# Optimization experiments

Hardware: AMD Instinct MI355X
Metric: run time of the kernel (lower is better)

Reference implementation:

```python
import jax, jax.numpy as jnp
import numpy as np
from jax import lax

B, T, C_IN, HW = 16, 2048, 17, 8
N_CONV, HID, OUT = 4, 150, 2
IN_SZ = N_CONV * 6 * 6  # 144


def setup_inputs() -> dict:
    key = jax.random.key(0)
    ks = jax.random.split(key, 9)
    s = lambda *sh: 1.0 / np.sqrt(sh[-1])
    return {
        "inputs": jax.random.normal(ks[0], (B, T, C_IN, HW, HW), jnp.float32),
        "conv_w": jax.random.normal(ks[1], (N_CONV, C_IN, 3, 3), jnp.float32) * 0.1,
        "conv_b": jax.random.normal(ks[2], (N_CONV,), jnp.float32) * 0.1,
        "w_ih": jax.random.normal(ks[3], (4 * HID, IN_SZ), jnp.float32) * s(IN_SZ),
        "w_hh": jax.random.normal(ks[4], (4 * HID, HID), jnp.float32) * s(HID),
        "b_ih": jax.random.normal(ks[5], (4 * HID,), jnp.float32) * s(HID),
        "b_hh": jax.random.normal(ks[6], (4 * HID,), jnp.float32) * s(HID),
        "last_w": jax.random.normal(ks[7], (OUT, HID), jnp.float32) * s(HID),
        "last_b": jax.random.normal(ks[8], (OUT,), jnp.float32) * s(HID),
    }


def reference(inputs, conv_w, conv_b, w_ih, w_hh, b_ih, b_hh, last_w, last_b):
    b, t = inputs.shape[:2]
    # Conv2d over all timesteps at once (same math as the per-step loop).
    x = inputs.reshape(b * t, C_IN, HW, HW)
    y = lax.conv_general_dilated(
        x, conv_w, window_strides=(1, 1), padding="VALID",
        dimension_numbers=("NCHW", "OIHW", "NCHW"),
    ) + conv_b[None, :, None, None]           # [B*T, 4, 6, 6]
    y = jax.nn.relu(y).reshape(b, t, IN_SZ)   # [B, T, 144]
    # Precompute input-to-gate projection for every step (batched GEMM).
    gates_x = jnp.einsum("btf,gf->btg", y, w_ih) + b_ih + b_hh  # [B, T, 600]

    def step(carry, gx):
        h, c = carry
        g = gx + h @ w_hh.T  # [B, 600]; PyTorch gate order: i, f, g, o
        i, f, gg, o = jnp.split(g, 4, axis=-1)
        c = jax.nn.sigmoid(f) * c + jax.nn.sigmoid(i) * jnp.tanh(gg)
        h = jax.nn.sigmoid(o) * jnp.tanh(c)
        return (h, c), None

    h0 = jnp.zeros((b, HID), inputs.dtype)
    (hT, _), _ = lax.scan(step, (h0, h0), jnp.swapaxes(gates_x, 0, 1))
    return hT @ last_w.T + last_b  # [B, 2] == last(h_T).squeeze()
```

## Files before the change

kernel.cpp:

```cpp
#include <hip/hip_runtime.h>

typedef _Float16 f16;
typedef _Float16 f16x4 __attribute__((ext_vector_type(4)));
typedef _Float16 f16x8 __attribute__((ext_vector_type(8)));
typedef float f32x4 __attribute__((ext_vector_type(4)));
typedef int i32x4 __attribute__((ext_vector_type(4)));

#define TLEN 2048
#define TPAD 2050
#define NCOL 640
#define GSTEP (16 * NCOL)
#define SPITCH 1100
#define K1 1.4426950408889634f
#define K2 2.8853900817779268f

__global__ __launch_bounds__(512, 1) void conv_gemm(
    const float* __restrict__ inp, const float* __restrict__ cw,
    const float* __restrict__ cb,
    const float* __restrict__ w_ih, const float* __restrict__ b_ih,
    const float* __restrict__ b_hh,
    f16* __restrict__ gates3)
{
    __shared__ __align__(16) float s_in[16][SPITCH];
    __shared__ __align__(16) f16 s_y[8][16][168];
    __shared__ float s_w[612];
    const int tid = threadIdx.x, w = tid >> 6, lane = tid & 63;
    const int col = lane & 15, grp = lane >> 4;
    for (int i = tid; i < 612; i += 512) s_w[i] = cw[i];

    f16x8 bfr[5][5];
    float bb[5];
    #pragma unroll
    for (int i = 0; i < 5; ++i) {
        const int colg = (w * 5 + i) * 16 + col;
        const int u = colg >> 2, G = colg & 3;
        const float sc = (G == 2) ? K2 : -K1;
        const bool valid = (u < 150);
        const int row = valid ? G * 150 + u : 0;
        #pragma unroll
        for (int kt = 0; kt < 5; ++kt) {
            const int k0 = kt * 32 + grp * 8;
            f16x8 v;
            #pragma unroll
            for (int e = 0; e < 8; ++e) v[e] = (f16)0.f;
            if (valid && k0 < 144) {
                const float* p = w_ih + (size_t)row * 144 + k0;
                #pragma unroll
                for (int e = 0; e < 8; ++e) v[e] = (f16)(p[e] * sc);
            }
            bfr[i][kt] = v;
        }
        bb[i] = valid ? (b_ih[row] + b_hh[row]) * sc : 0.f;
    }

    const int cb_b = tid & 15, unit = tid >> 4;
    const int oc = unit / 6, oy = unit % 6;
    const float cbias = (unit < 24) ? cb[oc] : 0.f;
    __syncthreads();

    const int t0 = blockIdx.x * 8;
    for (int tl = 0; tl < 8; ++tl) {
        const int t = t0 + tl;
        __syncthreads();
        {
            const int si = tid >> 5, l2 = tid & 31;
            const float4* ip =
                (const float4*)(inp + ((size_t)si * TLEN + t) * 1088);
            for (int k = l2; k < 272; k += 32)
                *(float4*)(&s_in[si][k * 4]) = ip[k];
        }
        __syncthreads();
        if (unit < 24) {
            const float* wp = s_w + oc * 153;
            float acc[6] = {cbias, cbias, cbias, cbias, cbias, cbias};
            #pragma unroll 1
            for (int ic = 0; ic < 17; ++ic) {
                #pragma unroll
                for (int ky = 0; ky < 3; ++ky) {
                    const float* r = &s_in[cb_b][ic * 64 + (oy + ky) * 8];
                    const float4 f0 = *(const float4*)r;
                    const float4 f1 = *(const float4*)(r + 4);
                    const float w0 = wp[ic * 9 + ky * 3 + 0];
                    const float w1 = wp[ic * 9 + ky * 3 + 1];
                    const float w2 = wp[ic * 9 + ky * 3 + 2];
                    acc[0] += f0.x * w0 + f0.y * w1 + f0.z * w2;
                    acc[1] += f0.y * w0 + f0.z * w1 + f0.w * w2;
                    acc[2] += f0.z * w0 + f0.w * w1 + f1.x * w2;
                    acc[3] += f0.w * w0 + f1.x * w1 + f1.y * w2;
                    acc[4] += f1.x * w0 + f1.y * w1 + f1.z * w2;
                    acc[5] += f1.y * w0 + f1.z * w1 + f1.w * w2;
                }
            }
            #pragma unroll
            for (int ox = 0; ox < 6; ++ox)
                s_y[tl][cb_b][oc * 36 + oy * 6 + ox] = (f16)fmaxf(acc[ox], 0.f);
        } else if (unit == 24) {
            #pragma unroll
            for (int k = 0; k < 16; ++k) s_y[tl][cb_b][144 + k] = (f16)0.f;
        }
    }
    __syncthreads();
    for (int tl = 0; tl < 8; ++tl) {
        const int t = t0 + tl;
        f16x8 a[5];
        #pragma unroll
        for (int kt = 0; kt < 5; ++kt)
            a[kt] = *(const f16x8*)(&s_y[tl][col][kt * 32 + grp * 8]);
        #pragma unroll
        for (int i = 0; i < 5; ++i) {
            f32x4 acc = {0.f, 0.f, 0.f, 0.f};
            #pragma unroll
            for (int kt = 0; kt < 5; ++kt)
                acc = __builtin_amdgcn_mfma_f32_16x16x32_f16(a[kt], bfr[i][kt], acc, 0, 0, 0);
            const int colg = (w * 5 + i) * 16 + col;
            #pragma unroll
            for (int r = 0; r < 4; ++r)
                gates3[((size_t)(t * 16 + grp * 4 + r)) * NCOL + colg] =
                    (f16)(acc[r] + bb[i]);
        }
    }
}

__device__ __forceinline__ void lstm_stepQ(
    int t, int cur, f16x4& pfu, f16x4& pfc, const f16*& pLoad,
    const i32x4 (&afrag)[5][3], const f32x4& scv,
    signed char* hqs, f16* hfs, float& cst,
    int grp, int sel, bool wr, int u)
{
    const f16x4 pnew = *(const f16x4*)pLoad;
    pLoad += GSTEP;

    const signed char* hr = hqs + cur * 192 + grp * 16;
    i32x4 bf[3];
    #pragma unroll
    for (int kt = 0; kt < 3; ++kt)
        bf[kt] = *(const i32x4*)(hr + kt * 64);

    float gx0 = (float)pfu[0], gx1 = (float)pfu[1];
    float gx2 = (float)pfu[2], gx3 = (float)pfu[3];
    pfc = pnew;

    const i32x4 zc = {0, 0, 0, 0};
    i32x4 acc[5];
    #pragma unroll
    for (int i = 0; i < 5; ++i)
        acc[i] = __builtin_amdgcn_mfma_i32_16x16x64_i8(afrag[i][0], bf[0], zc, 0, 0, 0);
    #pragma unroll
    for (int kt = 1; kt < 3; ++kt)
        #pragma unroll
        for (int i = 0; i < 5; ++i)
            acc[i] = __builtin_amdgcn_mfma_i32_16x16x64_i8(afrag[i][kt], bf[kt], acc[i], 0, 0, 0);

    int s0 = acc[0][0], s1 = acc[0][1], s2 = acc[0][2], s3 = acc[0][3];
    #pragma unroll
    for (int i = 1; i < 5; ++i) {
        const bool p = (sel == i);
        s0 = p ? acc[i][0] : s0;
        s1 = p ? acc[i][1] : s1;
        s2 = p ? acc[i][2] : s2;
        s3 = p ? acc[i][3] : s3;
    }

    const float g0 = fmaf((float)s0, scv[0], gx0);
    const float g1 = fmaf((float)s1, scv[1], gx1);
    const float g2 = fmaf((float)s2, scv[2], gx2);
    const float g3 = fmaf((float)s3, scv[3], gx3);

    const float ei = __builtin_amdgcn_exp2f(g0);
    const float ef = __builtin_amdgcn_exp2f(g1);
    const float eg = __builtin_amdgcn_exp2f(fminf(g2, 38.f));
    const float eo = __builtin_amdgcn_exp2f(g3);
    const float dig = (1.f + ei) * (eg + 1.f);
    const float c = cst * __builtin_amdgcn_rcpf(1.f + ef)
                  + (eg - 1.f) * __builtin_amdgcn_rcpf(dig);
    cst = c;
    const float ec = __builtin_amdgcn_exp2f(fminf(K2 * c, 80.f));
    const float h = (ec - 1.f) * __builtin_amdgcn_rcpf((1.f + eo) * (ec + 1.f));

    if (wr) hqs[(cur ^ 1) * 192 + u] = (signed char)(int)rintf(127.f * h);
    if (t == TLEN - 1 && wr) hfs[u] = (f16)h;

    asm volatile("s_waitcnt lgkmcnt(0)" ::: "memory");
    __builtin_amdgcn_s_barrier();
    __builtin_amdgcn_sched_barrier(0);
}

__global__ __launch_bounds__(512, 1) void lstm_scan(
    const f16* __restrict__ gates3, const float* __restrict__ w_hh,
    const float* __restrict__ last_w, const float* __restrict__ last_b,
    float* __restrict__ out)
{
    __shared__ __align__(16) signed char hq[2 * 192];
    __shared__ __align__(16) f16 hf[160];
    __shared__ float s_rm[600];
    const int b = blockIdx.x;
    const int tid = threadIdx.x, w = tid >> 6, lane = tid & 63;
    const int col = lane & 15, grp = lane >> 4;
    const int sel = (col < 5) ? col : ((col < 10) ? col - 5 : ((col < 15) ? col - 10 : 0));
    const bool wr = (col < 5);
    const int u = 20 * w + 4 * sel + grp;

    for (int i = tid; i < 2 * 192; i += 512) hq[i] = 0;

    for (int r = tid; r < 600; r += 512) {
        const float* p = w_hh + (size_t)r * 150;
        float m = 0.f;
        for (int k = 0; k < 150; k += 2) {
            m = fmaxf(m, fabsf(p[k]));
            m = fmaxf(m, fabsf(p[k + 1]));
        }
        s_rm[r] = m;
    }
    __syncthreads();

    i32x4 afrag[5][3];
    #pragma unroll
    for (int i = 0; i < 5; ++i) {
        const int colg = (5 * w + i) * 16 + col;
        const int uu = colg >> 2, G = colg & 3;
        const bool valid = (uu < 150);
        const int row = valid ? G * 150 + uu : 0;
        const float rm = s_rm[row];
        const float qs = (valid && rm > 0.f) ? 127.f / rm : 0.f;
        const float* p = w_hh + (size_t)row * 150;
        #pragma unroll
        for (int kt = 0; kt < 3; ++kt) {
            int wv[4] = {0, 0, 0, 0};
            #pragma unroll
            for (int byte = 0; byte < 16; ++byte) {
                const int k = kt * 64 + grp * 16 + byte;
                int q = 0;
                if (k < 150) q = (int)rintf(p[k] * qs);
                wv[byte >> 2] |= (q & 255) << ((byte & 3) * 8);
            }
            afrag[i][kt] = (i32x4){wv[0], wv[1], wv[2], wv[3]};
        }
    }
    f32x4 scv;
    {
        const bool vu = (u < 150);
        #pragma unroll
        for (int G = 0; G < 4; ++G) {
            const float sc = (G == 2) ? K2 : -K1;
            const int idx = vu ? G * 150 + u : 0;
            scv[G] = vu ? sc * s_rm[idx] * (1.f / 16129.f) : 0.f;
        }
    }
    float cst = 0.f;
    __syncthreads();

    const f16* gbu = gates3 + (size_t)b * NCOL + 80 * w + 16 * sel + 4 * grp;
    f16x4 pA = *(const f16x4*)(gbu);
    f16x4 pB = *(const f16x4*)(gbu + (size_t)1 * GSTEP);
    const f16* pLoad = gbu + (size_t)2 * GSTEP;

    #pragma unroll 1
    for (int tb = 0; tb < TLEN; tb += 2) {
        lstm_stepQ(tb,     0, pA, pA, pLoad, afrag, scv, hq, hf, cst, grp, sel, wr, u);
        lstm_stepQ(tb + 1, 1, pB, pB, pLoad, afrag, scv, hq, hf, cst, grp, sel, wr, u);
    }

    if (tid < 2) {
        float s = last_b[tid];
        for (int j = 0; j < 150; ++j)
            s += (float)hf[j] * last_w[tid * 150 + j];
        out[b * 2 + tid] = s;
    }
}

extern "C" void kernel_launch(void* const* d_in, const int* in_sizes, int n_in,
                              void* d_out, int out_size, void* d_ws, size_t ws_size,
                              hipStream_t stream) {
    const float* inp    = (const float*)d_in[0];
    const float* conv_w = (const float*)d_in[1];
    const float* conv_b = (const float*)d_in[2];
    const float* w_ih   = (const float*)d_in[3];
    const float* w_hh   = (const float*)d_in[4];
    const float* b_ih   = (const float*)d_in[5];
    const float* b_hh   = (const float*)d_in[6];
    const float* last_w = (const float*)d_in[7];
    const float* last_b = (const float*)d_in[8];
    float* out = (float*)d_out;

    f16* gates3 = (f16*)d_ws;

    conv_gemm<<<256, 512, 0, stream>>>(inp, conv_w, conv_b, w_ih, b_ih, b_hh, gates3);
    lstm_scan<<<16, 512, 0, stream>>>(gates3, w_hh, last_w, last_b, out);
}
```

Before: 1.004 ms.

## Merge conv-GEMM and LSTM scan into one persistent kernel with atomic handoff

Fuses the two launches into a single 256-block kernel. Blocks 16 and up act as producers that compute conv plus the input projection for 8–9 timesteps each, then bump a global counter. Blocks 0–15 run the LSTM scan: they quantize w_hh while the producers work, then spin on the counter until all 240 producers have finished. This hides the scan setup and the launch gap behind the conv phase. It relies on all 256 blocks being co-resident, adds a memset, and spreads the producer work over fewer blocks.

```diff
diff --git a/kernel.cpp b/kernel.cpp
--- a/kernel.cpp
+++ b/kernel.cpp
@@ -11,115 +11,9 @@
 #define NCOL 640
 #define GSTEP (16 * NCOL)
 #define SPITCH 1100
+#define NPROD 240
 #define K1 1.4426950408889634f
 #define K2 2.8853900817779268f
-
-__global__ __launch_bounds__(512, 1) void conv_gemm(
-    const float* __restrict__ inp, const float* __restrict__ cw,
-    const float* __restrict__ cb,
-    const float* __restrict__ w_ih, const float* __restrict__ b_ih,
-    const float* __restrict__ b_hh,
-    f16* __restrict__ gates3)
-{
-    __shared__ __align__(16) float s_in[16][SPITCH];
-    __shared__ __align__(16) f16 s_y[8][16][168];
-    __shared__ float s_w[612];
-    const int tid = threadIdx.x, w = tid >> 6, lane = tid & 63;
-    const int col = lane & 15, grp = lane >> 4;
-    for (int i = tid; i < 612; i += 512) s_w[i] = cw[i];
-
-    f16x8 bfr[5][5];
-    float bb[5];
-    #pragma unroll
-    for (int i = 0; i < 5; ++i) {
-        const int colg = (w * 5 + i) * 16 + col;
-        const int u = colg >> 2, G = colg & 3;
-        const float sc = (G == 2) ? K2 : -K1;
-        const bool valid = (u < 150);
-        const int row = valid ? G * 150 + u : 0;
-        #pragma unroll
-        for (int kt = 0; kt < 5; ++kt) {
-            const int k0 = kt * 32 + grp * 8;
-            f16x8 v;
-            #pragma unroll
-            for (int e = 0; e < 8; ++e) v[e] = (f16)0.f;
-            if (valid && k0 < 144) {
-                const float* p = w_ih + (size_t)row * 144 + k0;
-                #pragma unroll
-                for (int e = 0; e < 8; ++e) v[e] = (f16)(p[e] * sc);
-            }
-            bfr[i][kt] = v;
-        }
-        bb[i] = valid ? (b_ih[row] + b_hh[row]) * sc : 0.f;
-    }
-
-    const int cb_b = tid & 15, unit = tid >> 4;
-    const int oc = unit / 6, oy = unit % 6;
-    const float cbias = (unit < 24) ? cb[oc] : 0.f;
-    __syncthreads();
-
-    const int t0 = blockIdx.x * 8;
-    for (int tl = 0; tl < 8; ++tl) {
-        const int t = t0 + tl;
-        __syncthreads();
-        {
-            const int si = tid >> 5, l2 = tid & 31;
-            const float4* ip =
-                (const float4*)(inp + ((size_t)si * TLEN + t) * 1088);
-            for (int k = l2; k < 272; k += 32)
-                *(float4*)(&s_in[si][k * 4]) = ip[k];
-        }
-        __syncthreads();
-        if (unit < 24) {
-            const float* wp = s_w + oc * 153;
-            float acc[6] = {cbias, cbias, cbias, cbias, cbias, cbias};
-            #pragma unroll 1
-            for (int ic = 0; ic < 17; ++ic) {
-                #pragma unroll
-                for (int ky = 0; ky < 3; ++ky) {
-                    const float* r = &s_in[cb_b][ic * 64 + (oy + ky) * 8];
-                    const float4 f0 = *(const float4*)r;
-                    const float4 f1 = *(const float4*)(r + 4);
-                    const float w0 = wp[ic * 9 + ky * 3 + 0];
-                    const float w1 = wp[ic * 9 + ky * 3 + 1];
-                    const float w2 = wp[ic * 9 + ky * 3 + 2];
-                    acc[0] += f0.x * w0 + f0.y * w1 + f0.z * w2;
-                    acc[1] += f0.y * w0 + f0.z * w1 + f0.w * w2;
-                    acc[2] += f0.z * w0 + f0.w * w1 + f1.x * w2;
-                    acc[3] += f0.w * w0 + f1.x * w1 + f1.y * w2;
-                    acc[4] += f1.x * w0 + f1.y * w1 + f1.z * w2;
-                    acc[5] += f1.y * w0 + f1.z * w1 + f1.w * w2;
-                }
-            }
-            #pragma unroll
-            for (int ox = 0; ox < 6; ++ox)
-                s_y[tl][cb_b][oc * 36 + oy * 6 + ox] = (f16)fmaxf(acc[ox], 0.f);
-        } else if (unit == 24) {
-            #pragma unroll
-            for (int k = 0; k < 16; ++k) s_y[tl][cb_b][144 + k] = (f16)0.f;
-        }
-    }
-    __syncthreads();
-    for (int tl = 0; tl < 8; ++tl) {
-        const int t = t0 + tl;
-        f16x8 a[5];
-        #pragma unroll
-        for (int kt = 0; kt < 5; ++kt)
-            a[kt] = *(const f16x8*)(&s_y[tl][col][kt * 32 + grp * 8]);
-        #pragma unroll
-        for (int i = 0; i < 5; ++i) {
-            f32x4 acc = {0.f, 0.f, 0.f, 0.f};
-            #pragma unroll
-            for (int kt = 0; kt < 5; ++kt)
-                acc = __builtin_amdgcn_mfma_f32_16x16x32_f16(a[kt], bfr[i][kt], acc, 0, 0, 0);
-            const int colg = (w * 5 + i) * 16 + col;
-            #pragma unroll
-            for (int r = 0; r < 4; ++r)
-                gates3[((size_t)(t * 16 + grp * 4 + r)) * NCOL + colg] =
-                    (f16)(acc[r] + bb[i]);
-        }
-    }
-}
 
 __device__ __forceinline__ void lstm_stepQ(
     int t, int cur, f16x4& pfu, f16x4& pfc, const f16*& pLoad,
@@ -185,17 +79,128 @@
     __builtin_amdgcn_sched_barrier(0);
 }
 
-__global__ __launch_bounds__(512, 1) void lstm_scan(
-    const f16* __restrict__ gates3, const float* __restrict__ w_hh,
+__global__ __launch_bounds__(512, 1) void mega(
+    const float* __restrict__ inp, const float* __restrict__ cw,
+    const float* __restrict__ cb,
+    const float* __restrict__ w_ih, const float* __restrict__ b_ih,
+    const float* __restrict__ b_hh, const float* __restrict__ w_hh,
     const float* __restrict__ last_w, const float* __restrict__ last_b,
-    float* __restrict__ out)
+    f16* __restrict__ gates3, int* __restrict__ ctr, float* __restrict__ out)
 {
+    const int bid = blockIdx.x;
+    const int tid = threadIdx.x, w = tid >> 6, lane = tid & 63;
+    const int col = lane & 15, grp = lane >> 4;
+
+    if (bid >= 16) {
+        __shared__ __align__(16) float s_in[16][SPITCH];
+        __shared__ __align__(16) f16 s_y[16][168];
+        __shared__ float s_w[612];
+        for (int i = tid; i < 612; i += 512) s_w[i] = cw[i];
+
+        f16x8 bfr[5][5];
+        float bb[5];
+        #pragma unroll
+        for (int i = 0; i < 5; ++i) {
+            const int colg = (w * 5 + i) * 16 + col;
+            const int u = colg >> 2, G = colg & 3;
+            const float sc = (G == 2) ? K2 : -K1;
+            const bool valid = (u < 150);
+            const int row = valid ? G * 150 + u : 0;
+            #pragma unroll
+            for (int kt = 0; kt < 5; ++kt) {
+                const int k0 = kt * 32 + grp * 8;
+                f16x8 v;
+                #pragma unroll
+                for (int e = 0; e < 8; ++e) v[e] = (f16)0.f;
+                if (valid && k0 < 144) {
+                    const float* p = w_ih + (size_t)row * 144 + k0;
+                    #pragma unroll
+                    for (int e = 0; e < 8; ++e) v[e] = (f16)(p[e] * sc);
+                }
+                bfr[i][kt] = v;
+            }
+            bb[i] = valid ? (b_ih[row] + b_hh[row]) * sc : 0.f;
+        }
+
+        const int cb_b = tid & 15, unit = tid >> 4;
+        const int oc = unit / 6, oy = unit % 6;
+        const float cbias = (unit < 24) ? cb[oc] : 0.f;
+        __syncthreads();
+
+        const int idx = bid - 16;
+        const int tbeg = (idx < 128) ? idx * 9 : 1152 + (idx - 128) * 8;
+        const int tcnt = (idx < 128) ? 9 : 8;
+
+        for (int tl = 0; tl < tcnt; ++tl) {
+            const int t = tbeg + tl;
+            __syncthreads();
+            {
+                const int si = tid >> 5, l2 = tid & 31;
+                const float4* ip =
+                    (const float4*)(inp + ((size_t)si * TLEN + t) * 1088);
+                for (int k = l2; k < 272; k += 32)
+                    *(float4*)(&s_in[si][k * 4]) = ip[k];
+            }
+            __syncthreads();
+            if (unit < 24) {
+                const float* wp = s_w + oc * 153;
+                float acc[6] = {cbias, cbias, cbias, cbias, cbias, cbias};
+                #pragma unroll 1
+                for (int ic = 0; ic < 17; ++ic) {
+                    #pragma unroll
+                    for (int ky = 0; ky < 3; ++ky) {
+                        const float* r = &s_in[cb_b][ic * 64 + (oy + ky) * 8];
+                        const float4 f0 = *(const float4*)r;
+                        const float4 f1 = *(const float4*)(r + 4);
+                        const float w0 = wp[ic * 9 + ky * 3 + 0];
+                        const float w1 = wp[ic * 9 + ky * 3 + 1];
+                        const float w2 = wp[ic * 9 + ky * 3 + 2];
+                        acc[0] += f0.x * w0 + f0.y * w1 + f0.z * w2;
+                        acc[1] += f0.y * w0 + f0.z * w1 + f0.w * w2;
+                        acc[2] += f0.z * w0 + f0.w * w1 + f1.x * w2;
+                        acc[3] += f0.w * w0 + f1.x * w1 + f1.y * w2;
+                        acc[4] += f1.x * w0 + f1.y * w1 + f1.z * w2;
+                        acc[5] += f1.y * w0 + f1.z * w1 + f1.w * w2;
+                    }
+                }
+                #pragma unroll
+                for (int ox = 0; ox < 6; ++ox)
+                    s_y[cb_b][oc * 36 + oy * 6 + ox] = (f16)fmaxf(acc[ox], 0.f);
+            } else if (unit == 24) {
+                #pragma unroll
+                for (int k = 0; k < 16; ++k) s_y[cb_b][144 + k] = (f16)0.f;
+            }
+            __syncthreads();
+            f16x8 a[5];
+            #pragma unroll
+            for (int kt = 0; kt < 5; ++kt)
+                a[kt] = *(const f16x8*)(&s_y[col][kt * 32 + grp * 8]);
+            #pragma unroll
+            for (int i = 0; i < 5; ++i) {
+                f32x4 acc = {0.f, 0.f, 0.f, 0.f};
+                #pragma unroll
+                for (int kt = 0; kt < 5; ++kt)
+                    acc = __builtin_amdgcn_mfma_f32_16x16x32_f16(a[kt], bfr[i][kt], acc, 0, 0, 0);
+                const int colg = (w * 5 + i) * 16 + col;
+                #pragma unroll
+                for (int r = 0; r < 4; ++r)
+                    gates3[((size_t)(t * 16 + grp * 4 + r)) * NCOL + colg] =
+                        (f16)(acc[r] + bb[i]);
+            }
+        }
+
+        __threadfence();
+        __syncthreads();
+        if (tid == 0)
+            __hip_atomic_fetch_add(ctr, 1, __ATOMIC_RELEASE,
+                                   __HIP_MEMORY_SCOPE_AGENT);
+        return;
+    }
+
     __shared__ __align__(16) signed char hq[2 * 192];
     __shared__ __align__(16) f16 hf[160];
     __shared__ float s_rm[600];
-    const int b = blockIdx.x;
-    const int tid = threadIdx.x, w = tid >> 6, lane = tid & 63;
-    const int col = lane & 15, grp = lane >> 4;
+    const int b = bid;
     const int sel = (col < 5) ? col : ((col < 10) ? col - 5 : ((col < 15) ? col - 10 : 0));
     const bool wr = (col < 5);
     const int u = 20 * w + 4 * sel + grp;
@@ -242,11 +247,18 @@
         #pragma unroll
         for (int G = 0; G < 4; ++G) {
             const float sc = (G == 2) ? K2 : -K1;
-            const int idx = vu ? G * 150 + u : 0;
-            scv[G] = vu ? sc * s_rm[idx] * (1.f / 16129.f) : 0.f;
+            const int idx2 = vu ? G * 150 + u : 0;
+            scv[G] = vu ? sc * s_rm[idx2] * (1.f / 16129.f) : 0.f;
         }
     }
     float cst = 0.f;
+    __syncthreads();
+
+    if (tid == 0) {
+        while (__hip_atomic_load(ctr, __ATOMIC_ACQUIRE,
+                                 __HIP_MEMORY_SCOPE_AGENT) < NPROD)
+            __builtin_amdgcn_s_sleep(8);
+    }
     __syncthreads();
 
     const f16* gbu = gates3 + (size_t)b * NCOL + 80 * w + 16 * sel + 4 * grp;
@@ -282,8 +294,11 @@
     const float* last_b = (const float*)d_in[8];
     float* out = (float*)d_out;
 
-    f16* gates3 = (f16*)d_ws;
-
-    conv_gemm<<<256, 512, 0, stream>>>(inp, conv_w, conv_b, w_ih, b_ih, b_hh, gates3);
-    lstm_scan<<<16, 512, 0, stream>>>(gates3, w_hh, last_w, last_b, out);
+    char* ws = (char*)d_ws;
+    f16* gates3 = (f16*)ws;
+    int* ctr    = (int*)(ws + 41984000);
+
+    hipMemsetAsync(ctr, 0, 64, stream);
+    mega<<<256, 512, 0, stream>>>(inp, conv_w, conv_b, w_ih, b_ih, b_hh, w_hh,
+                                  last_w, last_b, gates3, ctr, out);
 }
```

Result: slower. 1.077 ms (+7.2%).
